# Kernel optimization log

Measured on AMD Instinct MI355X. Metric: run time of the kernel, lower is better.

## Reference

```python
import jax, jax.numpy as jnp
import numpy as np

B, T, HID, H = 2, 2048, 2048, 8
DK, DV = 256, 512          # head_qk_dim, head_v_dim
CHUNK = 64                 # chunk size used by fused_chunk retention
EPS = 1e-5


def setup_inputs() -> dict:
    key = jax.random.key(0)
    ks = jax.random.split(key, 7)
    s = 0.02  # ~ xavier_uniform with gain 2**-2.5
    return {
        "hidden_states": jax.random.normal(ks[0], (B, T, HID), jnp.float32),
        "Wq": jax.random.normal(ks[1], (HID, H * DK), jnp.float32) * s,
        "Wk": jax.random.normal(ks[2], (HID, H * DK), jnp.float32) * s,
        "Wv": jax.random.normal(ks[3], (HID, H * DV), jnp.float32) * s,
        "Wg": jax.random.normal(ks[4], (HID, H * DV), jnp.float32) * s,
        "Wo": jax.random.normal(ks[5], (H * DV, HID), jnp.float32) * s,
        "g_norm_w": jnp.ones((DV,), jnp.float32),
    }


def _rotary(x):
    # x: [B, T, H, D], non-interleaved rotary over full head dim, base 10000
    d = x.shape[-1]
    inv = 1.0 / (10000.0 ** (jnp.arange(0, d, 2, dtype=jnp.float32) / d))
    fr = jnp.arange(x.shape[1], dtype=jnp.float32)[:, None] * inv  # [T, d/2]
    cos = jnp.cos(fr)[None, :, None, :]
    sin = jnp.sin(fr)[None, :, None, :]
    x1, x2 = jnp.split(x, 2, axis=-1)
    return jnp.concatenate([x1 * cos - x2 * sin, x2 * cos + x1 * sin], axis=-1)


def _retention(q, k, v):
    # q,k: [B,H,T,DK]; v: [B,H,T,DV]; per-head decay gamma_h = 1 - 2^(-5-h)
    gamma = 1.0 - jnp.exp2(-5.0 - jnp.arange(H, dtype=jnp.float32))  # [H]
    q = q * (DK ** -0.5)
    N = T // CHUNK
    qc = q.reshape(B, H, N, CHUNK, DK).transpose(2, 0, 1, 3, 4)  # [N,B,H,C,K]
    kc = k.reshape(B, H, N, CHUNK, DK).transpose(2, 0, 1, 3, 4)
    vc = v.reshape(B, H, N, CHUNK, DV).transpose(2, 0, 1, 3, 4)
    i = jnp.arange(CHUNK, dtype=jnp.float32)
    # intra-chunk causal decay matrix D[h,i,j] = gamma_h^(i-j) for i>=j else 0
    Dm = jnp.where(i[:, None] >= i[None, :],
                   gamma[:, None, None] ** (i[:, None] - i[None, :]), 0.0)  # [H,C,C]
    qd = gamma[:, None] ** (i + 1.0)            # [H,C]: decay applied to q vs carried state
    kd = gamma[:, None] ** (CHUNK - 1.0 - i)    # [H,C]: decay applied to k for state update
    gC = gamma ** CHUNK                          # [H]

    def step(S, qkv):
        qcu, kcu, vcu = qkv  # [B,H,C,K], [B,H,C,K], [B,H,C,V]
        A = jnp.einsum('bhik,bhjk->bhij', qcu, kcu) * Dm[None]
        o_intra = jnp.einsum('bhij,bhjv->bhiv', A, vcu)
        o_inter = jnp.einsum('bhck,bhkv->bhcv', qcu * qd[None, :, :, None], S)
        kv = jnp.einsum('bhck,bhcv->bhkv', kcu * kd[None, :, :, None], vcu)
        S_new = gC[None, :, None, None] * S + kv
        return S_new, o_intra + o_inter

    S0 = jnp.zeros((B, H, DK, DV), jnp.float32)
    _, o = jax.lax.scan(step, S0, (qc, kc, vc))  # o: [N,B,H,C,V]
    return o.transpose(1, 2, 0, 3, 4).reshape(B, H, T, DV)


def reference(hidden_states, Wq, Wk, Wv, Wg, Wo, g_norm_w):
    q = (hidden_states @ Wq).reshape(B, T, H, DK)
    k = (hidden_states @ Wk).reshape(B, T, H, DK)
    v = (hidden_states @ Wv).reshape(B, T, H, DV)
    q = _rotary(q)
    k = _rotary(k)
    o = _retention(q.transpose(0, 2, 1, 3), k.transpose(0, 2, 1, 3),
                   v.transpose(0, 2, 1, 3))          # [B,H,T,DV]
    o = o.transpose(0, 2, 1, 3)                       # [B,T,H,DV]
    g = (hidden_states @ Wg).reshape(B, T, H, DV)
    # fused RMSNorm (per head_v_dim) + swish gate
    o = o * jax.lax.rsqrt(jnp.mean(o * o, axis=-1, keepdims=True) + EPS) * g_norm_w
    o = o * (g * jax.nn.sigmoid(g))
    return o.reshape(B, T, H * DV) @ Wo
```

## Files before the change

### kernel.cpp

```cpp
#include <hip/hip_runtime.h>
#include <cstdint>
#include <cstddef>

typedef __bf16 bf16;
typedef __bf16 bf16x8 __attribute__((ext_vector_type(8)));
typedef float  f32x4  __attribute__((ext_vector_type(4)));

#define MFMA16(a, b, c) __builtin_amdgcn_mfma_f32_16x16x32_bf16((a), (b), (c), 0, 0, 0)

__device__ __forceinline__ void async16(const bf16* g, bf16* l) {
  __builtin_amdgcn_global_load_lds(
      (const __attribute__((address_space(1))) unsigned int*)g,
      (__attribute__((address_space(3))) unsigned int*)l, 16, 0, 0);
}

__global__ __launch_bounds__(256) void k_cast(const float* __restrict__ x, bf16* __restrict__ y) {
  size_t i = ((size_t)blockIdx.x * 256 + threadIdx.x) * 4;
  float4 a = *(const float4*)(x + i);
  union { bf16 h[4]; uint2 u; } pk;
  pk.h[0] = (bf16)a.x; pk.h[1] = (bf16)a.y; pk.h[2] = (bf16)a.z; pk.h[3] = (bf16)a.w;
  *(uint2*)(y + i) = pk.u;
}

__global__ __launch_bounds__(256) void k_transpose_cast(const float* __restrict__ W,
                                                        bf16* __restrict__ WT, int K, int N) {
  __shared__ float tile[32][33];
  int k0 = blockIdx.y << 5, n0 = blockIdx.x << 5;
  int r = threadIdx.x >> 5, c = threadIdx.x & 31;
#pragma unroll
  for (int p = 0; p < 4; p++)
    tile[r + p * 8][c] = W[(size_t)(k0 + r + p * 8) * N + n0 + c];
  __syncthreads();
#pragma unroll
  for (int p = 0; p < 4; p++) {
    int nn = r + p * 8;
    WT[(size_t)(n0 + nn) * K + k0 + c] = (bf16)tile[c][nn];
  }
}

template <int OUT_BF16>
__global__ __launch_bounds__(256) void k_gemm_bt(const bf16* __restrict__ A,
                                                 const bf16* __restrict__ Bt,
                                                 void* __restrict__ C, int M, int N, int K) {
  __shared__ bf16 a_lds[128 * 64];
  __shared__ bf16 b_lds[128 * 64];
  int tid = threadIdx.x;
  int wave = tid >> 6, lane = tid & 63, quad = lane >> 4, l16 = lane & 15;
  int wr = wave >> 1, wc = wave & 1;
  int m0 = blockIdx.y << 7, n0 = blockIdx.x << 7;
  f32x4 acc[4][4] = {};
  const bf16* ag = A + (size_t)(m0 + (tid >> 3)) * K + (tid & 7) * 8;
  const bf16* bg = Bt + (size_t)(n0 + (tid >> 3)) * K + (tid & 7) * 8;
  bf16* al = a_lds + wave * 512;
  bf16* bl = b_lds + wave * 512;
  for (int kt = 0; kt < K; kt += 64) {
#pragma unroll
    for (int i = 0; i < 4; i++) {
      async16(ag + (size_t)i * 32 * K, al + i * 2048);
      async16(bg + (size_t)i * 32 * K, bl + i * 2048);
    }
    ag += 64; bg += 64;
    __syncthreads();
#pragma unroll
    for (int kk = 0; kk < 2; kk++) {
      bf16x8 af[4], bfv[4];
#pragma unroll
      for (int mt = 0; mt < 4; mt++)
        af[mt] = *(const bf16x8*)&a_lds[(wr * 64 + mt * 16 + l16) * 64 + kk * 32 + quad * 8];
#pragma unroll
      for (int nt = 0; nt < 4; nt++)
        bfv[nt] = *(const bf16x8*)&b_lds[(wc * 64 + nt * 16 + l16) * 64 + kk * 32 + quad * 8];
#pragma unroll
      for (int mt = 0; mt < 4; mt++)
#pragma unroll
        for (int nt = 0; nt < 4; nt++)
          acc[mt][nt] = MFMA16(af[mt], bfv[nt], acc[mt][nt]);
    }
    __syncthreads();
  }
#pragma unroll
  for (int mt = 0; mt < 4; mt++)
#pragma unroll
    for (int nt = 0; nt < 4; nt++)
#pragma unroll
      for (int r = 0; r < 4; r++) {
        int row = m0 + wr * 64 + mt * 16 + quad * 4 + r;
        int col = n0 + wc * 64 + nt * 16 + l16;
        if (OUT_BF16)
          ((bf16*)C)[(size_t)row * N + col] = (bf16)acc[mt][nt][r];
        else
          ((float*)C)[(size_t)row * N + col] = acc[mt][nt][r];
      }
}

__global__ __launch_bounds__(256) void k_rotary(bf16* __restrict__ x, float scale) {
  int tid = threadIdx.x;
  int row = blockIdx.x * 2 + (tid >> 7);
  int j = tid & 127;
  int t = (row >> 3) & 2047;
  float inv = exp2f(-0.10381025296522976f * (float)j);
  float ang = (float)t * inv;
  float s, c;
  sincosf(ang, &s, &c);
  size_t base = (size_t)row * 256;
  float x1 = (float)x[base + j], x2 = (float)x[base + j + 128];
  x[base + j]       = (bf16)((x1 * c - x2 * s) * scale);
  x[base + j + 128] = (bf16)((x2 * c + x1 * s) * scale);
}

__global__ __launch_bounds__(256) void k_retention(const bf16* __restrict__ q,
                                                   const bf16* __restrict__ k,
                                                   const bf16* __restrict__ v,
                                                   float* __restrict__ o0,
                                                   float* __restrict__ o1) {
  __shared__ bf16 q_lds[64][136];
  __shared__ bf16 k_lds[64][136];
  __shared__ bf16 St_lds[64][136];
  __shared__ bf16 kt_lds[128][88];
  __shared__ bf16 vt_lds[64][88];
  __shared__ bf16 v2t_lds[64][88];
  __shared__ bf16 A_lds[64][88];

  int gid = blockIdx.x;
  int kh = gid & 1, vb = (gid >> 1) & 7, h = (gid >> 4) & 7, b = gid >> 7;
  float* oout = kh ? o1 : o0;
  int tid = threadIdx.x, lane = tid & 63, wave = tid >> 6, quad = lane >> 4, l16 = lane & 15;
  int wr = wave >> 1, wc = wave & 1;
  float gamma = 1.f - exp2f(-5.f - (float)h);
  float lg = log2f(gamma);
  float gC = exp2f(64.f * lg);

  f32x4 S[8];
#pragma unroll
  for (int i = 0; i < 8; i++) S[i] = (f32x4){0.f, 0.f, 0.f, 0.f};

  for (int n = 0; n < 32; n++) {
    int t0 = n * 64;
    __syncthreads();
#pragma unroll
    for (int a = 0; a < 2; a++)
#pragma unroll
      for (int bb = 0; bb < 4; bb++) {
        int k0 = wave * 32 + a * 16 + quad * 4;
        int vc = bb * 16 + l16;
        f32x4 s = S[a * 4 + bb];
        union { bf16 hh[4]; unsigned long long u; } pk;
        pk.hh[0] = (bf16)s[0]; pk.hh[1] = (bf16)s[1];
        pk.hh[2] = (bf16)s[2]; pk.hh[3] = (bf16)s[3];
        *(unsigned long long*)&St_lds[vc][k0] = pk.u;
      }
#pragma unroll
    for (int p = 0; p < 4; p++) {
      int c = p * 16 + (tid >> 4);
      int ko = (tid & 15) * 8;
      const bf16* src = q + (((size_t)(b * 2048 + t0 + c) * 8 + h) << 8) + kh * 128 + ko;
      *(uint4*)&q_lds[c][ko] = *(const uint4*)src;
    }
#pragma unroll
    for (int p = 0; p < 4; p++) {
      int c = p * 16 + (tid >> 4);
      int ko = (tid & 15) * 8;
      const bf16* src = k + (((size_t)(b * 2048 + t0 + c) * 8 + h) << 8) + kh * 128 + ko;
      uint4 d = *(const uint4*)src;
      *(uint4*)&k_lds[c][ko] = d;
      const bf16* e = (const bf16*)&d;
#pragma unroll
      for (int j = 0; j < 8; j++) kt_lds[ko + j][c] = e[j];
    }
#pragma unroll
    for (int p = 0; p < 2; p++) {
      int c = p * 32 + (tid >> 3);
      int jo = (tid & 7) * 8;
      const bf16* src = v + ((size_t)(b * 2048 + t0 + c)) * 4096 + h * 512 + vb * 64 + jo;
      uint4 d = *(const uint4*)src;
      const bf16* e = (const bf16*)&d;
      float kd = exp2f(lg * (float)(63 - c));
#pragma unroll
      for (int j = 0; j < 8; j++) {
        vt_lds[jo + j][c] = e[j];
        v2t_lds[jo + j][c] = (bf16)(kd * (float)e[j]);
      }
    }
    __syncthreads();
#pragma unroll
    for (int it = 0; it < 2; it++) {
      int ar = wr * 32 + it * 16 + l16;
      bf16x8 af[4];
#pragma unroll
      for (int kk = 0; kk < 4; kk++) af[kk] = *(const bf16x8*)&q_lds[ar][kk * 32 + quad * 8];
#pragma unroll
      for (int jt = 0; jt < 2; jt++) {
        int br = wc * 32 + jt * 16 + l16;
        f32x4 aacc = (f32x4){0.f, 0.f, 0.f, 0.f};
#pragma unroll
        for (int kk = 0; kk < 4; kk++) {
          bf16x8 bfv = *(const bf16x8*)&k_lds[br][kk * 32 + quad * 8];
          aacc = MFMA16(af[kk], bfv, aacc);
        }
        int i0 = wr * 32 + it * 16 + quad * 4;
        int j = wc * 32 + jt * 16 + l16;
#pragma unroll
        for (int r = 0; r < 4; r++) {
          int d = i0 + r - j;
          float val = (d >= 0) ? aacc[r] * exp2f(lg * (float)d) : 0.f;
          A_lds[i0 + r][j] = (bf16)val;
        }
      }
    }
    __syncthreads();
    f32x4 oacc[2][2];
    oacc[0][0] = (f32x4){0.f, 0.f, 0.f, 0.f}; oacc[0][1] = (f32x4){0.f, 0.f, 0.f, 0.f};
    oacc[1][0] = (f32x4){0.f, 0.f, 0.f, 0.f}; oacc[1][1] = (f32x4){0.f, 0.f, 0.f, 0.f};
#pragma unroll
    for (int mt = 0; mt < 2; mt++) {
      int ar = wr * 32 + mt * 16 + l16;
      bf16x8 af[4];
#pragma unroll
      for (int kk = 0; kk < 4; kk++) af[kk] = *(const bf16x8*)&q_lds[ar][kk * 32 + quad * 8];
#pragma unroll
      for (int nt = 0; nt < 2; nt++) {
        int br = wc * 32 + nt * 16 + l16;
#pragma unroll
        for (int kk = 0; kk < 4; kk++) {
          bf16x8 bfv = *(const bf16x8*)&St_lds[br][kk * 32 + quad * 8];
          oacc[mt][nt] = MFMA16(af[kk], bfv, oacc[mt][nt]);
        }
      }
    }
#pragma unroll
    for (int mt = 0; mt < 2; mt++) {
      int i0 = wr * 32 + mt * 16 + quad * 4;
#pragma unroll
      for (int r = 0; r < 4; r++) {
        float qd = exp2f(lg * (float)(i0 + r + 1));
        oacc[mt][0][r] *= qd;
        oacc[mt][1][r] *= qd;
      }
    }
    {
      bf16x8 bfr[2][2];
#pragma unroll
      for (int nt = 0; nt < 2; nt++)
#pragma unroll
        for (int kk = 0; kk < 2; kk++)
          bfr[nt][kk] = *(const bf16x8*)&vt_lds[wc * 32 + nt * 16 + l16][kk * 32 + quad * 8];
#pragma unroll
      for (int mt = 0; mt < 2; mt++) {
        bf16x8 af2[2];
#pragma unroll
        for (int kk = 0; kk < 2; kk++)
          af2[kk] = *(const bf16x8*)&A_lds[wr * 32 + mt * 16 + l16][kk * 32 + quad * 8];
#pragma unroll
        for (int nt = 0; nt < 2; nt++)
#pragma unroll
          for (int kk = 0; kk < 2; kk++)
            oacc[mt][nt] = MFMA16(af2[kk], bfr[nt][kk], oacc[mt][nt]);
      }
    }
#pragma unroll
    for (int mt = 0; mt < 2; mt++)
#pragma unroll
      for (int nt = 0; nt < 2; nt++)
#pragma unroll
        for (int r = 0; r < 4; r++) {
          int rowt = t0 + wr * 32 + mt * 16 + quad * 4 + r;
          int col = vb * 64 + wc * 32 + nt * 16 + l16;
          oout[(((size_t)(b * 2048 + rowt)) * 8 + h) * 512 + col] = oacc[mt][nt][r];
        }
    {
      bf16x8 bfr[4][2];
#pragma unroll
      for (int bb = 0; bb < 4; bb++)
#pragma unroll
        for (int kk = 0; kk < 2; kk++)
          bfr[bb][kk] = *(const bf16x8*)&v2t_lds[bb * 16 + l16][kk * 32 + quad * 8];
#pragma unroll
      for (int a = 0; a < 2; a++) {
        bf16x8 af3[2];
#pragma unroll
        for (int kk = 0; kk < 2; kk++)
          af3[kk] = *(const bf16x8*)&kt_lds[wave * 32 + a * 16 + l16][kk * 32 + quad * 8];
#pragma unroll
        for (int bb = 0; bb < 4; bb++) {
          f32x4 cc = S[a * 4 + bb] * gC;
#pragma unroll
          for (int kk = 0; kk < 2; kk++) cc = MFMA16(af3[kk], bfr[bb][kk], cc);
          S[a * 4 + bb] = cc;
        }
      }
    }
  }
}

__global__ __launch_bounds__(256) void k_normgate(const float* __restrict__ o0,
                                                  const float* __restrict__ o1,
                                                  const bf16* __restrict__ g,
                                                  const float* __restrict__ gw,
                                                  bf16* __restrict__ og) {
  int tid = threadIdx.x, lane = tid & 63;
  size_t row = (size_t)blockIdx.x * 4 + (tid >> 6);
  size_t base = row * 512;
  float vv[8];
  float ss = 0.f;
#pragma unroll
  for (int hh = 0; hh < 2; hh++) {
    int col = hh * 256 + lane * 4;
    float4 a = *(const float4*)(o0 + base + col);
    float4 b = *(const float4*)(o1 + base + col);
    vv[hh * 4 + 0] = a.x + b.x; vv[hh * 4 + 1] = a.y + b.y;
    vv[hh * 4 + 2] = a.z + b.z; vv[hh * 4 + 3] = a.w + b.w;
#pragma unroll
    for (int jj = 0; jj < 4; jj++) ss += vv[hh * 4 + jj] * vv[hh * 4 + jj];
  }
#pragma unroll
  for (int off = 1; off < 64; off <<= 1) ss += __shfl_xor(ss, off, 64);
  float rinv = rsqrtf(ss * (1.0f / 512.0f) + 1e-5f);
#pragma unroll
  for (int hh = 0; hh < 2; hh++) {
    int col = hh * 256 + lane * 4;
    union { bf16 h[4]; uint2 u; } gp;
    gp.u = *(const uint2*)(g + base + col);
    union { bf16 h[4]; uint2 u; } op;
#pragma unroll
    for (int jj = 0; jj < 4; jj++) {
      float gg = (float)gp.h[jj];
      float y = vv[hh * 4 + jj] * rinv * gw[col + jj] * (gg / (1.f + expf(-gg)));
      op.h[jj] = (bf16)y;
    }
    *(uint2*)(og + base + col) = op.u;
  }
}

extern "C" void kernel_launch(void* const* d_in, const int* in_sizes, int n_in,
                              void* d_out, int out_size, void* d_ws, size_t ws_size,
                              hipStream_t stream) {
  (void)in_sizes; (void)n_in; (void)out_size; (void)ws_size;
  const float* hs = (const float*)d_in[0];
  const float* Wq = (const float*)d_in[1];
  const float* Wk = (const float*)d_in[2];
  const float* Wv = (const float*)d_in[3];
  const float* Wg = (const float*)d_in[4];
  const float* Wo = (const float*)d_in[5];
  const float* gw = (const float*)d_in[6];
  float* out = (float*)d_out;

  char* ws = (char*)d_ws;
  const size_t MB = 1024 * 1024;
  bf16* hid = (bf16*)(ws + 0);
  bf16* WqT = (bf16*)(ws + 16 * MB);
  bf16* WkT = (bf16*)(ws + 24 * MB);
  bf16* WvT = (bf16*)(ws + 32 * MB);
  bf16* WgT = (bf16*)(ws + 48 * MB);
  bf16* qb  = (bf16*)(ws + 64 * MB);
  bf16* kb  = (bf16*)(ws + 80 * MB);
  bf16* vbuf= (bf16*)(ws + 96 * MB);
  bf16* gb  = (bf16*)(ws + 128 * MB);
  float* o0 = (float*)(ws + 0);
  bf16* og  = (bf16*)(ws + 64 * MB);
  bf16* WoT = (bf16*)(ws + 96 * MB);
  float* o1 = (float*)(ws + 160 * MB);

  k_cast<<<8192, 256, 0, stream>>>(hs, hid);
  k_transpose_cast<<<dim3(64, 64), 256, 0, stream>>>(Wq, WqT, 2048, 2048);
  k_transpose_cast<<<dim3(64, 64), 256, 0, stream>>>(Wk, WkT, 2048, 2048);
  k_transpose_cast<<<dim3(128, 64), 256, 0, stream>>>(Wv, WvT, 2048, 4096);
  k_transpose_cast<<<dim3(128, 64), 256, 0, stream>>>(Wg, WgT, 2048, 4096);

  k_gemm_bt<1><<<dim3(16, 32), 256, 0, stream>>>(hid, WqT, qb, 4096, 2048, 2048);
  k_gemm_bt<1><<<dim3(16, 32), 256, 0, stream>>>(hid, WkT, kb, 4096, 2048, 2048);
  k_gemm_bt<1><<<dim3(32, 32), 256, 0, stream>>>(hid, WvT, vbuf, 4096, 4096, 2048);
  k_gemm_bt<1><<<dim3(32, 32), 256, 0, stream>>>(hid, WgT, gb, 4096, 4096, 2048);

  k_rotary<<<16384, 256, 0, stream>>>(qb, 0.0625f);
  k_rotary<<<16384, 256, 0, stream>>>(kb, 1.0f);

  k_retention<<<256, 256, 0, stream>>>(qb, kb, vbuf, o0, o1);

  k_transpose_cast<<<dim3(64, 128), 256, 0, stream>>>(Wo, WoT, 4096, 2048);
  k_normgate<<<8192, 256, 0, stream>>>(o0, o1, gb, gw, og);
  k_gemm_bt<0><<<dim3(16, 32), 256, 0, stream>>>(og, WoT, out, 4096, 2048, 4096);
}
```

Before: 781.4 us.

## Double-buffer retention staging, fuse QKVG GEMMs, fold k decay into rotary

The retention kernel now loads q, k and pre-transposed kT/vT tiles into double-buffered LDS with async global-to-LDS copies, so the next chunk's loads overlap the current chunk's compute. The intra-chunk score matrix stays in registers and is reshuffled with ds_bpermute instead of a round trip through LDS. The per-position k decay is folded into the rotary pass, so the intra-chunk and state-update terms share one scaled k. The four projection GEMMs become one launch over a concatenated weight matrix, and retention partial outputs are written in bf16 to halve traffic into the norm/gate kernel. The cost is two extra transpose kernels for k and v and some added bf16 rounding of the outputs.

After: 784.9 us. Within noise of the previous version (+0.4%).

```diff
diff --git a/kernel.cpp b/kernel.cpp
--- a/kernel.cpp
+++ b/kernel.cpp
@@ -38,10 +38,27 @@
   }
 }
 
-template <int OUT_BF16>
-__global__ __launch_bounds__(256) void k_gemm_bt(const bf16* __restrict__ A,
-                                                 const bf16* __restrict__ Bt,
-                                                 void* __restrict__ C, int M, int N, int K) {
+__global__ __launch_bounds__(256) void k_transpose_bh(const bf16* __restrict__ src,
+                                                      bf16* __restrict__ dst, int D) {
+  __shared__ bf16 tile[32][33];
+  int bh = blockIdx.z;
+  int b = bh >> 3, h = bh & 7;
+  int d0 = blockIdx.x << 5, t0 = blockIdx.y << 5;
+  int r = threadIdx.x >> 5, c = threadIdx.x & 31;
+#pragma unroll
+  for (int p = 0; p < 4; p++)
+    tile[r + p * 8][c] = src[((size_t)((b * 2048 + t0 + r + p * 8) * 8 + h)) * D + d0 + c];
+  __syncthreads();
+#pragma unroll
+  for (int p = 0; p < 4; p++)
+    dst[((size_t)(bh * D + d0 + r + p * 8)) * 2048 + t0 + c] = tile[c][r + p * 8];
+}
+
+__global__ __launch_bounds__(256) void k_gemm_qkvg(const bf16* __restrict__ A,
+                                                   const bf16* __restrict__ Bt,
+                                                   bf16* __restrict__ qb, bf16* __restrict__ kb,
+                                                   bf16* __restrict__ vbuf, bf16* __restrict__ gb) {
+  const int K = 2048;
   __shared__ bf16 a_lds[128 * 64];
   __shared__ bf16 b_lds[128 * 64];
   int tid = threadIdx.x;
@@ -78,6 +95,62 @@
     }
     __syncthreads();
   }
+  bf16* dst; int ldd, c0;
+  if (n0 < 2048)       { dst = qb;   ldd = 2048; c0 = n0; }
+  else if (n0 < 4096)  { dst = kb;   ldd = 2048; c0 = n0 - 2048; }
+  else if (n0 < 8192)  { dst = vbuf; ldd = 4096; c0 = n0 - 4096; }
+  else                 { dst = gb;   ldd = 4096; c0 = n0 - 8192; }
+#pragma unroll
+  for (int mt = 0; mt < 4; mt++)
+#pragma unroll
+    for (int nt = 0; nt < 4; nt++)
+#pragma unroll
+      for (int r = 0; r < 4; r++) {
+        int row = m0 + wr * 64 + mt * 16 + quad * 4 + r;
+        int col = c0 + wc * 64 + nt * 16 + l16;
+        dst[(size_t)row * ldd + col] = (bf16)acc[mt][nt][r];
+      }
+}
+
+__global__ __launch_bounds__(256) void k_gemm_bt(const bf16* __restrict__ A,
+                                                 const bf16* __restrict__ Bt,
+                                                 float* __restrict__ C, int M, int N, int K) {
+  __shared__ bf16 a_lds[128 * 64];
+  __shared__ bf16 b_lds[128 * 64];
+  int tid = threadIdx.x;
+  int wave = tid >> 6, lane = tid & 63, quad = lane >> 4, l16 = lane & 15;
+  int wr = wave >> 1, wc = wave & 1;
+  int m0 = blockIdx.y << 7, n0 = blockIdx.x << 7;
+  f32x4 acc[4][4] = {};
+  const bf16* ag = A + (size_t)(m0 + (tid >> 3)) * K + (tid & 7) * 8;
+  const bf16* bg = Bt + (size_t)(n0 + (tid >> 3)) * K + (tid & 7) * 8;
+  bf16* al = a_lds + wave * 512;
+  bf16* bl = b_lds + wave * 512;
+  for (int kt = 0; kt < K; kt += 64) {
+#pragma unroll
+    for (int i = 0; i < 4; i++) {
+      async16(ag + (size_t)i * 32 * K, al + i * 2048);
+      async16(bg + (size_t)i * 32 * K, bl + i * 2048);
+    }
+    ag += 64; bg += 64;
+    __syncthreads();
+#pragma unroll
+    for (int kk = 0; kk < 2; kk++) {
+      bf16x8 af[4], bfv[4];
+#pragma unroll
+      for (int mt = 0; mt < 4; mt++)
+        af[mt] = *(const bf16x8*)&a_lds[(wr * 64 + mt * 16 + l16) * 64 + kk * 32 + quad * 8];
+#pragma unroll
+      for (int nt = 0; nt < 4; nt++)
+        bfv[nt] = *(const bf16x8*)&b_lds[(wc * 64 + nt * 16 + l16) * 64 + kk * 32 + quad * 8];
+#pragma unroll
+      for (int mt = 0; mt < 4; mt++)
+#pragma unroll
+        for (int nt = 0; nt < 4; nt++)
+          acc[mt][nt] = MFMA16(af[mt], bfv[nt], acc[mt][nt]);
+    }
+    __syncthreads();
+  }
 #pragma unroll
   for (int mt = 0; mt < 4; mt++)
 #pragma unroll
@@ -86,18 +159,21 @@
       for (int r = 0; r < 4; r++) {
         int row = m0 + wr * 64 + mt * 16 + quad * 4 + r;
         int col = n0 + wc * 64 + nt * 16 + l16;
-        if (OUT_BF16)
-          ((bf16*)C)[(size_t)row * N + col] = (bf16)acc[mt][nt][r];
-        else
-          ((float*)C)[(size_t)row * N + col] = acc[mt][nt][r];
-      }
-}
-
-__global__ __launch_bounds__(256) void k_rotary(bf16* __restrict__ x, float scale) {
+        C[(size_t)row * N + col] = acc[mt][nt][r];
+      }
+}
+
+__global__ __launch_bounds__(256) void k_rotary(bf16* __restrict__ x, float qscale, int kmode) {
   int tid = threadIdx.x;
   int row = blockIdx.x * 2 + (tid >> 7);
   int j = tid & 127;
   int t = (row >> 3) & 2047;
+  int h = row & 7;
+  float scale = qscale;
+  if (kmode) {
+    float lg = log2f(1.f - exp2f(-5.f - (float)h));
+    scale = exp2f(lg * (float)(63 - (t & 63)));
+  }
   float inv = exp2f(-0.10381025296522976f * (float)j);
   float ang = (float)t * inv;
   float s, c;
@@ -110,190 +186,180 @@
 
 __global__ __launch_bounds__(256) void k_retention(const bf16* __restrict__ q,
                                                    const bf16* __restrict__ k,
-                                                   const bf16* __restrict__ v,
-                                                   float* __restrict__ o0,
-                                                   float* __restrict__ o1) {
-  __shared__ bf16 q_lds[64][136];
-  __shared__ bf16 k_lds[64][136];
-  __shared__ bf16 St_lds[64][136];
-  __shared__ bf16 kt_lds[128][88];
-  __shared__ bf16 vt_lds[64][88];
-  __shared__ bf16 v2t_lds[64][88];
-  __shared__ bf16 A_lds[64][88];
+                                                   const bf16* __restrict__ kT,
+                                                   const bf16* __restrict__ vT,
+                                                   bf16* __restrict__ o0,
+                                                   bf16* __restrict__ o1) {
+  __shared__ bf16 qA[2][64 * 128];
+  __shared__ bf16 kA[2][64 * 128];
+  __shared__ bf16 ktA[2][128 * 64];
+  __shared__ bf16 vtA[2][64 * 64];
+  __shared__ bf16 StA[2][64 * 136];
 
   int gid = blockIdx.x;
   int kh = gid & 1, vb = (gid >> 1) & 7, h = (gid >> 4) & 7, b = gid >> 7;
-  float* oout = kh ? o1 : o0;
+  bf16* oout = kh ? o1 : o0;
   int tid = threadIdx.x, lane = tid & 63, wave = tid >> 6, quad = lane >> 4, l16 = lane & 15;
-  int wr = wave >> 1, wc = wave & 1;
   float gamma = 1.f - exp2f(-5.f - (float)h);
   float lg = log2f(gamma);
   float gC = exp2f(64.f * lg);
-
-  f32x4 S[8];
-#pragma unroll
-  for (int i = 0; i < 8; i++) S[i] = (f32x4){0.f, 0.f, 0.f, 0.f};
+  int iRow = wave * 16 + l16;
+  float ei = exp2f(lg * (float)(iRow - 63));
+  float qd[4];
+#pragma unroll
+  for (int r = 0; r < 4; r++) qd[r] = exp2f(lg * (float)(wave * 16 + quad * 4 + r + 1));
+
+  f32x4 S[2][4];
+#pragma unroll
+  for (int a = 0; a < 2; a++)
+#pragma unroll
+    for (int bb = 0; bb < 4; bb++) S[a][bb] = (f32x4){0.f, 0.f, 0.f, 0.f};
+
+  auto stage = [&](int t0, int p) {
+#pragma unroll 1
+    for (int s = wave; s < 56; s += 4) {
+      if (s < 16) {
+        int i = s, c = i * 4 + (lane >> 4), off = (lane & 15) * 8;
+        async16(q + (((size_t)((b * 2048 + t0 + c) * 8 + h)) << 8) + kh * 128 + off,
+                &qA[p][i * 512]);
+      } else if (s < 32) {
+        int i = s - 16, c = i * 4 + (lane >> 4), off = (lane & 15) * 8;
+        async16(k + (((size_t)((b * 2048 + t0 + c) * 8 + h)) << 8) + kh * 128 + off,
+                &kA[p][i * 512]);
+      } else if (s < 48) {
+        int i = s - 32, kd = i * 8 + (lane >> 3), off = (lane & 7) * 8;
+        async16(kT + ((size_t)((b * 8 + h) * 256 + kh * 128 + kd)) * 2048 + t0 + off,
+                &ktA[p][i * 512]);
+      } else {
+        int i = s - 48, vd = i * 8 + (lane >> 3), off = (lane & 7) * 8;
+        async16(vT + ((size_t)((b * 8 + h) * 512 + vb * 64 + vd)) * 2048 + t0 + off,
+                &vtA[p][i * 512]);
+      }
+    }
+  };
+
+  stage(0, 0);
 
   for (int n = 0; n < 32; n++) {
-    int t0 = n * 64;
-    __syncthreads();
+    int p = n & 1, t0 = n * 64;
 #pragma unroll
     for (int a = 0; a < 2; a++)
 #pragma unroll
       for (int bb = 0; bb < 4; bb++) {
         int k0 = wave * 32 + a * 16 + quad * 4;
         int vc = bb * 16 + l16;
-        f32x4 s = S[a * 4 + bb];
-        union { bf16 hh[4]; unsigned long long u; } pk;
-        pk.hh[0] = (bf16)s[0]; pk.hh[1] = (bf16)s[1];
-        pk.hh[2] = (bf16)s[2]; pk.hh[3] = (bf16)s[3];
-        *(unsigned long long*)&St_lds[vc][k0] = pk.u;
-      }
-#pragma unroll
-    for (int p = 0; p < 4; p++) {
-      int c = p * 16 + (tid >> 4);
-      int ko = (tid & 15) * 8;
-      const bf16* src = q + (((size_t)(b * 2048 + t0 + c) * 8 + h) << 8) + kh * 128 + ko;
-      *(uint4*)&q_lds[c][ko] = *(const uint4*)src;
-    }
-#pragma unroll
-    for (int p = 0; p < 4; p++) {
-      int c = p * 16 + (tid >> 4);
-      int ko = (tid & 15) * 8;
-      const bf16* src = k + (((size_t)(b * 2048 + t0 + c) * 8 + h) << 8) + kh * 128 + ko;
-      uint4 d = *(const uint4*)src;
-      *(uint4*)&k_lds[c][ko] = d;
-      const bf16* e = (const bf16*)&d;
-#pragma unroll
-      for (int j = 0; j < 8; j++) kt_lds[ko + j][c] = e[j];
-    }
-#pragma unroll
-    for (int p = 0; p < 2; p++) {
-      int c = p * 32 + (tid >> 3);
-      int jo = (tid & 7) * 8;
-      const bf16* src = v + ((size_t)(b * 2048 + t0 + c)) * 4096 + h * 512 + vb * 64 + jo;
-      uint4 d = *(const uint4*)src;
-      const bf16* e = (const bf16*)&d;
-      float kd = exp2f(lg * (float)(63 - c));
-#pragma unroll
-      for (int j = 0; j < 8; j++) {
-        vt_lds[jo + j][c] = e[j];
-        v2t_lds[jo + j][c] = (bf16)(kd * (float)e[j]);
-      }
-    }
+        f32x4 s = S[a][bb];
+        union { bf16 hh[4]; unsigned long long u; } pkk;
+        pkk.hh[0] = (bf16)s[0]; pkk.hh[1] = (bf16)s[1];
+        pkk.hh[2] = (bf16)s[2]; pkk.hh[3] = (bf16)s[3];
+        *(unsigned long long*)&StA[p][vc * 136 + k0] = pkk.u;
+      }
     __syncthreads();
-#pragma unroll
-    for (int it = 0; it < 2; it++) {
-      int ar = wr * 32 + it * 16 + l16;
-      bf16x8 af[4];
-#pragma unroll
-      for (int kk = 0; kk < 4; kk++) af[kk] = *(const bf16x8*)&q_lds[ar][kk * 32 + quad * 8];
-#pragma unroll
-      for (int jt = 0; jt < 2; jt++) {
-        int br = wc * 32 + jt * 16 + l16;
-        f32x4 aacc = (f32x4){0.f, 0.f, 0.f, 0.f};
-#pragma unroll
-        for (int kk = 0; kk < 4; kk++) {
-          bf16x8 bfv = *(const bf16x8*)&k_lds[br][kk * 32 + quad * 8];
-          aacc = MFMA16(af[kk], bfv, aacc);
-        }
-        int i0 = wr * 32 + it * 16 + quad * 4;
-        int j = wc * 32 + jt * 16 + l16;
-#pragma unroll
-        for (int r = 0; r < 4; r++) {
-          int d = i0 + r - j;
-          float val = (d >= 0) ? aacc[r] * exp2f(lg * (float)d) : 0.f;
-          A_lds[i0 + r][j] = (bf16)val;
-        }
-      }
-    }
-    __syncthreads();
-    f32x4 oacc[2][2];
-    oacc[0][0] = (f32x4){0.f, 0.f, 0.f, 0.f}; oacc[0][1] = (f32x4){0.f, 0.f, 0.f, 0.f};
-    oacc[1][0] = (f32x4){0.f, 0.f, 0.f, 0.f}; oacc[1][1] = (f32x4){0.f, 0.f, 0.f, 0.f};
-#pragma unroll
-    for (int mt = 0; mt < 2; mt++) {
-      int ar = wr * 32 + mt * 16 + l16;
-      bf16x8 af[4];
-#pragma unroll
-      for (int kk = 0; kk < 4; kk++) af[kk] = *(const bf16x8*)&q_lds[ar][kk * 32 + quad * 8];
-#pragma unroll
-      for (int nt = 0; nt < 2; nt++) {
-        int br = wc * 32 + nt * 16 + l16;
-#pragma unroll
-        for (int kk = 0; kk < 4; kk++) {
-          bf16x8 bfv = *(const bf16x8*)&St_lds[br][kk * 32 + quad * 8];
-          oacc[mt][nt] = MFMA16(af[kk], bfv, oacc[mt][nt]);
-        }
-      }
-    }
-#pragma unroll
-    for (int mt = 0; mt < 2; mt++) {
-      int i0 = wr * 32 + mt * 16 + quad * 4;
+    if (n < 31) stage(t0 + 64, 1 - p);
+
+    bf16x8 qf[4];
+#pragma unroll
+    for (int kk = 0; kk < 4; kk++)
+      qf[kk] = *(const bf16x8*)&qA[p][iRow * 128 + kk * 32 + quad * 8];
+
+    f32x4 Dt[4];
+#pragma unroll
+    for (int jt = 0; jt < 4; jt++) {
+      Dt[jt] = (f32x4){0.f, 0.f, 0.f, 0.f};
+#pragma unroll
+      for (int kk = 0; kk < 4; kk++) {
+        bf16x8 kf = *(const bf16x8*)&kA[p][(jt * 16 + l16) * 128 + kk * 32 + quad * 8];
+        Dt[jt] = MFMA16(kf, qf[kk], Dt[jt]);
+      }
+    }
+    unsigned pkA[4][2];
+#pragma unroll
+    for (int jt = 0; jt < 4; jt++) {
+      int j0 = jt * 16 + quad * 4;
+      union { bf16 hh[2]; unsigned u; } p0, p1;
+      p0.hh[0] = (bf16)((iRow >= j0 + 0) ? Dt[jt][0] * ei : 0.f);
+      p0.hh[1] = (bf16)((iRow >= j0 + 1) ? Dt[jt][1] * ei : 0.f);
+      p1.hh[0] = (bf16)((iRow >= j0 + 2) ? Dt[jt][2] * ei : 0.f);
+      p1.hh[1] = (bf16)((iRow >= j0 + 3) ? Dt[jt][3] * ei : 0.f);
+      pkA[jt][0] = p0.u; pkA[jt][1] = p1.u;
+    }
+    int s0b = ((((quad & 1) << 5) + l16) << 2);
+    int s1b = s0b + 64;
+    bool hi = (quad >> 1) != 0;
+    bf16x8 afA[2];
+#pragma unroll
+    for (int kk = 0; kk < 2; kk++) {
+      unsigned x00 = __builtin_amdgcn_ds_bpermute(s0b, (int)pkA[2 * kk][0]);
+      unsigned x01 = __builtin_amdgcn_ds_bpermute(s0b, (int)pkA[2 * kk][1]);
+      unsigned x10 = __builtin_amdgcn_ds_bpermute(s0b, (int)pkA[2 * kk + 1][0]);
+      unsigned x11 = __builtin_amdgcn_ds_bpermute(s0b, (int)pkA[2 * kk + 1][1]);
+      unsigned y00 = __builtin_amdgcn_ds_bpermute(s1b, (int)pkA[2 * kk][0]);
+      unsigned y01 = __builtin_amdgcn_ds_bpermute(s1b, (int)pkA[2 * kk][1]);
+      unsigned y10 = __builtin_amdgcn_ds_bpermute(s1b, (int)pkA[2 * kk + 1][0]);
+      unsigned y11 = __builtin_amdgcn_ds_bpermute(s1b, (int)pkA[2 * kk + 1][1]);
+      union { unsigned u[4]; bf16x8 v; } rr;
+      rr.u[0] = hi ? x10 : x00;
+      rr.u[1] = hi ? x11 : x01;
+      rr.u[2] = hi ? y10 : y00;
+      rr.u[3] = hi ? y11 : y01;
+      afA[kk] = rr.v;
+    }
+
+    f32x4 oacc[4];
+#pragma unroll
+    for (int nt = 0; nt < 4; nt++) {
+      oacc[nt] = (f32x4){0.f, 0.f, 0.f, 0.f};
+#pragma unroll
+      for (int kk = 0; kk < 4; kk++) {
+        bf16x8 stf = *(const bf16x8*)&StA[p][(nt * 16 + l16) * 136 + kk * 32 + quad * 8];
+        oacc[nt] = MFMA16(qf[kk], stf, oacc[nt]);
+      }
+    }
+#pragma unroll
+    for (int nt = 0; nt < 4; nt++)
+#pragma unroll
+      for (int r = 0; r < 4; r++) oacc[nt][r] *= qd[r];
+
+    bf16x8 vtf[4][2];
+#pragma unroll
+    for (int nt = 0; nt < 4; nt++)
+#pragma unroll
+      for (int kk = 0; kk < 2; kk++)
+        vtf[nt][kk] = *(const bf16x8*)&vtA[p][(nt * 16 + l16) * 64 + kk * 32 + quad * 8];
+#pragma unroll
+    for (int nt = 0; nt < 4; nt++)
+#pragma unroll
+      for (int kk = 0; kk < 2; kk++)
+        oacc[nt] = MFMA16(afA[kk], vtf[nt][kk], oacc[nt]);
+
+#pragma unroll
+    for (int nt = 0; nt < 4; nt++)
 #pragma unroll
       for (int r = 0; r < 4; r++) {
-        float qd = exp2f(lg * (float)(i0 + r + 1));
-        oacc[mt][0][r] *= qd;
-        oacc[mt][1][r] *= qd;
-      }
-    }
-    {
-      bf16x8 bfr[2][2];
-#pragma unroll
-      for (int nt = 0; nt < 2; nt++)
-#pragma unroll
-        for (int kk = 0; kk < 2; kk++)
-          bfr[nt][kk] = *(const bf16x8*)&vt_lds[wc * 32 + nt * 16 + l16][kk * 32 + quad * 8];
-#pragma unroll
-      for (int mt = 0; mt < 2; mt++) {
-        bf16x8 af2[2];
-#pragma unroll
-        for (int kk = 0; kk < 2; kk++)
-          af2[kk] = *(const bf16x8*)&A_lds[wr * 32 + mt * 16 + l16][kk * 32 + quad * 8];
-#pragma unroll
-        for (int nt = 0; nt < 2; nt++)
-#pragma unroll
-          for (int kk = 0; kk < 2; kk++)
-            oacc[mt][nt] = MFMA16(af2[kk], bfr[nt][kk], oacc[mt][nt]);
-      }
-    }
-#pragma unroll
-    for (int mt = 0; mt < 2; mt++)
-#pragma unroll
-      for (int nt = 0; nt < 2; nt++)
-#pragma unroll
-        for (int r = 0; r < 4; r++) {
-          int rowt = t0 + wr * 32 + mt * 16 + quad * 4 + r;
-          int col = vb * 64 + wc * 32 + nt * 16 + l16;
-          oout[(((size_t)(b * 2048 + rowt)) * 8 + h) * 512 + col] = oacc[mt][nt][r];
-        }
-    {
-      bf16x8 bfr[4][2];
-#pragma unroll
-      for (int bb = 0; bb < 4; bb++)
-#pragma unroll
-        for (int kk = 0; kk < 2; kk++)
-          bfr[bb][kk] = *(const bf16x8*)&v2t_lds[bb * 16 + l16][kk * 32 + quad * 8];
-#pragma unroll
-      for (int a = 0; a < 2; a++) {
-        bf16x8 af3[2];
-#pragma unroll
-        for (int kk = 0; kk < 2; kk++)
-          af3[kk] = *(const bf16x8*)&kt_lds[wave * 32 + a * 16 + l16][kk * 32 + quad * 8];
-#pragma unroll
-        for (int bb = 0; bb < 4; bb++) {
-          f32x4 cc = S[a * 4 + bb] * gC;
-#pragma unroll
-          for (int kk = 0; kk < 2; kk++) cc = MFMA16(af3[kk], bfr[bb][kk], cc);
-          S[a * 4 + bb] = cc;
-        }
-      }
-    }
-  }
-}
-
-__global__ __launch_bounds__(256) void k_normgate(const float* __restrict__ o0,
-                                                  const float* __restrict__ o1,
+        int row = t0 + wave * 16 + quad * 4 + r;
+        int col = vb * 64 + nt * 16 + l16;
+        oout[((size_t)((b * 2048 + row) * 8 + h)) * 512 + col] = (bf16)oacc[nt][r];
+      }
+
+#pragma unroll
+    for (int a = 0; a < 2; a++) {
+      bf16x8 ktf[2];
+#pragma unroll
+      for (int kk = 0; kk < 2; kk++)
+        ktf[kk] = *(const bf16x8*)&ktA[p][(wave * 32 + a * 16 + l16) * 64 + kk * 32 + quad * 8];
+#pragma unroll
+      for (int bb = 0; bb < 4; bb++) {
+        f32x4 cc = S[a][bb] * gC;
+#pragma unroll
+        for (int kk = 0; kk < 2; kk++) cc = MFMA16(ktf[kk], vtf[bb][kk], cc);
+        S[a][bb] = cc;
+      }
+    }
+  }
+}
+
+__global__ __launch_bounds__(256) void k_normgate(const bf16* __restrict__ o0,
+                                                  const bf16* __restrict__ o1,
                                                   const bf16* __restrict__ g,
                                                   const float* __restrict__ gw,
                                                   bf16* __restrict__ og) {
@@ -305,12 +371,15 @@
 #pragma unroll
   for (int hh = 0; hh < 2; hh++) {
     int col = hh * 256 + lane * 4;
-    float4 a = *(const float4*)(o0 + base + col);
-    float4 b = *(const float4*)(o1 + base + col);
-    vv[hh * 4 + 0] = a.x + b.x; vv[hh * 4 + 1] = a.y + b.y;
-    vv[hh * 4 + 2] = a.z + b.z; vv[hh * 4 + 3] = a.w + b.w;
-#pragma unroll
-    for (int jj = 0; jj < 4; jj++) ss += vv[hh * 4 + jj] * vv[hh * 4 + jj];
+    union { bf16 h[4]; uint2 u; } a, b2;
+    a.u = *(const uint2*)(o0 + base + col);
+    b2.u = *(const uint2*)(o1 + base + col);
+#pragma unroll
+    for (int jj = 0; jj < 4; jj++) {
+      float v = (float)a.h[jj] + (float)b2.h[jj];
+      vv[hh * 4 + jj] = v;
+      ss += v * v;
+    }
   }
 #pragma unroll
   for (int off = 1; off < 64; off <<= 1) ss += __shfl_xor(ss, off, 64);
@@ -347,36 +416,35 @@
   char* ws = (char*)d_ws;
   const size_t MB = 1024 * 1024;
   bf16* hid = (bf16*)(ws + 0);
-  bf16* WqT = (bf16*)(ws + 16 * MB);
-  bf16* WkT = (bf16*)(ws + 24 * MB);
-  bf16* WvT = (bf16*)(ws + 32 * MB);
-  bf16* WgT = (bf16*)(ws + 48 * MB);
+  bf16* WT  = (bf16*)(ws + 16 * MB);
   bf16* qb  = (bf16*)(ws + 64 * MB);
   bf16* kb  = (bf16*)(ws + 80 * MB);
   bf16* vbuf= (bf16*)(ws + 96 * MB);
   bf16* gb  = (bf16*)(ws + 128 * MB);
-  float* o0 = (float*)(ws + 0);
-  bf16* og  = (bf16*)(ws + 64 * MB);
-  bf16* WoT = (bf16*)(ws + 96 * MB);
-  float* o1 = (float*)(ws + 160 * MB);
+  bf16* kT  = (bf16*)(ws + 160 * MB);
+  bf16* vT  = (bf16*)(ws + 176 * MB);
+  bf16* o0  = (bf16*)(ws + 0);
+  bf16* o1  = (bf16*)(ws + 32 * MB);
+  bf16* og  = (bf16*)(ws + 160 * MB);
+  bf16* WoT = (bf16*)(ws + 192 * MB);
 
   k_cast<<<8192, 256, 0, stream>>>(hs, hid);
-  k_transpose_cast<<<dim3(64, 64), 256, 0, stream>>>(Wq, WqT, 2048, 2048);
-  k_transpose_cast<<<dim3(64, 64), 256, 0, stream>>>(Wk, WkT, 2048, 2048);
-  k_transpose_cast<<<dim3(128, 64), 256, 0, stream>>>(Wv, WvT, 2048, 4096);
-  k_transpose_cast<<<dim3(128, 64), 256, 0, stream>>>(Wg, WgT, 2048, 4096);
-
-  k_gemm_bt<1><<<dim3(16, 32), 256, 0, stream>>>(hid, WqT, qb, 4096, 2048, 2048);
-  k_gemm_bt<1><<<dim3(16, 32), 256, 0, stream>>>(hid, WkT, kb, 4096, 2048, 2048);
-  k_gemm_bt<1><<<dim3(32, 32), 256, 0, stream>>>(hid, WvT, vbuf, 4096, 4096, 2048);
-  k_gemm_bt<1><<<dim3(32, 32), 256, 0, stream>>>(hid, WgT, gb, 4096, 4096, 2048);
-
-  k_rotary<<<16384, 256, 0, stream>>>(qb, 0.0625f);
-  k_rotary<<<16384, 256, 0, stream>>>(kb, 1.0f);
-
-  k_retention<<<256, 256, 0, stream>>>(qb, kb, vbuf, o0, o1);
+  k_transpose_cast<<<dim3(64, 64), 256, 0, stream>>>(Wq, WT, 2048, 2048);
+  k_transpose_cast<<<dim3(64, 64), 256, 0, stream>>>(Wk, WT + (size_t)2048 * 2048, 2048, 2048);
+  k_transpose_cast<<<dim3(128, 64), 256, 0, stream>>>(Wv, WT + (size_t)4096 * 2048, 2048, 4096);
+  k_transpose_cast<<<dim3(128, 64), 256, 0, stream>>>(Wg, WT + (size_t)8192 * 2048, 2048, 4096);
+
+  k_gemm_qkvg<<<dim3(96, 32), 256, 0, stream>>>(hid, WT, qb, kb, vbuf, gb);
+
+  k_rotary<<<16384, 256, 0, stream>>>(qb, 0.0625f, 0);
+  k_rotary<<<16384, 256, 0, stream>>>(kb, 1.0f, 1);
+
+  k_transpose_bh<<<dim3(8, 64, 16), 256, 0, stream>>>(kb, kT, 256);
+  k_transpose_bh<<<dim3(16, 64, 16), 256, 0, stream>>>(vbuf, vT, 512);
+
+  k_retention<<<256, 256, 0, stream>>>(qb, kb, kT, vT, o0, o1);
 
   k_transpose_cast<<<dim3(64, 128), 256, 0, stream>>>(Wo, WoT, 4096, 2048);
   k_normgate<<<8192, 256, 0, stream>>>(o0, o1, gb, gw, og);
-  k_gemm_bt<0><<<dim3(16, 32), 256, 0, stream>>>(og, WoT, out, 4096, 2048, 4096);
-}
+  k_gemm_bt<<<dim3(16, 32), 256, 0, stream>>>(og, WoT, out, 4096, 2048, 4096);
+}
```
